# Kernel tuning notes

Hardware: AMD Instinct MI355X
Metric: run time of the kernel (lower is better)

The kernel has to match this reference:

```python
import jax, jax.numpy as jnp
import numpy as np

N_NODES = 100_000
N_EDGES = 1_600_000
IN_FEATS = 64
H_DIMS = 64
OUT_A = 2
OUT_B = 21
N_LAYERS = 2
EPS = 1e-5


def setup_inputs() -> dict:
    key = jax.random.key(0)
    ks = jax.random.split(key, 16)
    d = H_DIMS

    def rn(k, shape, scale=0.05):
        return jax.random.normal(k, shape, dtype=jnp.float32) * scale

    return {
        "v": jax.random.normal(ks[0], (N_NODES, IN_FEATS), dtype=jnp.float32),
        "src": jax.random.randint(ks[1], (N_EDGES,), 0, N_NODES),
        "dst": jax.random.randint(ks[2], (N_EDGES,), 0, N_NODES),
        "rel_type": jax.random.randint(ks[3], (N_EDGES,), 0, 3),
        "norm": jax.random.uniform(ks[4], (N_EDGES,), dtype=jnp.float32),
        "emb_W": rn(ks[5], (d, IN_FEATS)),
        "emb_b": jnp.zeros((d,), jnp.float32),
        "emb_gamma": jnp.ones((d,), jnp.float32),
        "emb_beta": jnp.zeros((d,), jnp.float32),
        "rel_weight": rn(ks[6], (3, d, d)),
        "gru_Wih": rn(ks[7], (3 * d, d)),
        "gru_Whh": rn(ks[8], (3 * d, d)),
        "gru_bih": jnp.zeros((3 * d,), jnp.float32),
        "gru_bhh": jnp.zeros((3 * d,), jnp.float32),
        "ker_gamma": jnp.ones((d,), jnp.float32),
        "ker_beta": jnp.zeros((d,), jnp.float32),
        "a_W1": rn(ks[9], (d, d)), "a_b1": jnp.zeros((d,), jnp.float32),
        "a_gamma": jnp.ones((d,), jnp.float32), "a_beta": jnp.zeros((d,), jnp.float32),
        "a_W2": rn(ks[10], (OUT_A, d)), "a_b2": jnp.zeros((OUT_A,), jnp.float32),
        "b_W1": rn(ks[11], (d, d)), "b_b1": jnp.zeros((d,), jnp.float32),
        "b_gamma": jnp.ones((d,), jnp.float32), "b_beta": jnp.zeros((d,), jnp.float32),
        "b_W2": rn(ks[12], (OUT_B, d)), "b_b2": jnp.zeros((OUT_B,), jnp.float32),
    }


def _bn(x, gamma, beta):
    # BatchNorm1d in training mode: batch statistics, biased variance
    mu = jnp.mean(x, axis=0)
    var = jnp.var(x, axis=0)
    return (x - mu) * jax.lax.rsqrt(var + EPS) * gamma + beta


def _gru_cell(x, h, Wih, Whh, bih, bhh):
    # torch nn.GRU single layer, gate order (r, z, n)
    gi = x @ Wih.T + bih
    gh = h @ Whh.T + bhh
    ir, iz, inn = jnp.split(gi, 3, axis=-1)
    hr, hz, hn = jnp.split(gh, 3, axis=-1)
    r = jax.nn.sigmoid(ir + hr)
    z = jax.nn.sigmoid(iz + hz)
    n = jnp.tanh(inn + r * hn)
    return (1.0 - z) * n + z * h


def reference(v, src, dst, rel_type, norm, emb_W, emb_b, emb_gamma, emb_beta,
              rel_weight, gru_Wih, gru_Whh, gru_bih, gru_bhh, ker_gamma, ker_beta,
              a_W1, a_b1, a_gamma, a_beta, a_W2, a_b2,
              b_W1, b_b1, b_gamma, b_beta, b_W2, b_b2):
    # Embedding: Linear -> BN -> ReLU
    h0 = jax.nn.relu(_bn(v @ emb_W.T + emb_b, emb_gamma, emb_beta))
    output = h0
    h = jnp.zeros_like(h0)
    n_nodes = v.shape[0]
    for _ in range(N_LAYERS):
        # per-node relational transform for all 3 relations: [N, 3, d]
        x3 = jnp.einsum('nd,rdk->nrk', output, rel_weight)
        msg = x3[src, rel_type] * norm[:, None]                     # [E, d]
        swh = jax.ops.segment_sum(msg, dst, num_segments=n_nodes)   # [N, d]
        h = _gru_cell(swh, h, gru_Wih, gru_Whh, gru_bih, gru_bhh)
        output = h
    hk = _bn(output, ker_gamma, ker_beta)
    # task heads: Linear -> BN -> ReLU -> Linear (MLP with h_layers=2)
    xa = jax.nn.relu(_bn(hk @ a_W1.T + a_b1, a_gamma, a_beta)) @ a_W2.T + a_b2
    xb = jax.nn.relu(_bn(hk @ b_W1.T + b_b1, b_gamma, b_beta)) @ b_W2.T + b_b2
    return xa, xb
```

## Files before the change

### kernel.cpp

```cpp
#include <hip/hip_runtime.h>

#define NN 100000
#define NE 1600000
#define NP 100096
#define NBKT 391
#define CAP 6144
#define EPSV 1e-5f

typedef unsigned int u32;
typedef unsigned short u16;
typedef unsigned long long u64;
typedef __bf16 bf16x8 __attribute__((ext_vector_type(8)));
typedef float f32x4 __attribute__((ext_vector_type(4)));

#define GLBP(x) ((const __attribute__((address_space(1))) u32*)(x))
#define LDSP(x) ((__attribute__((address_space(3))) u32*)(x))

__device__ __forceinline__ u16 f2bf(float f) {
  u32 x = __float_as_uint(f);
  return (u16)((x + 0x7FFFu + ((x >> 16) & 1u)) >> 16);
}
__device__ __forceinline__ float bf2f(u16 h) { return __uint_as_float(((u32)h) << 16); }

__device__ __forceinline__ void pack_one(const float* W, u32* out, int K, int KOT, int i) {
  int q = i & 3, lane = (i >> 2) & 63, f = i >> 8;
  int ks = f / KOT, ot = f - ks * KOT;
  int o = ot * 16 + (lane & 15);
  int k = ks * 32 + (lane >> 4) * 8 + q * 2;
  out[i] = (u32)f2bf(W[o * K + k]) | ((u32)f2bf(W[o * K + k + 1]) << 16);
}

__global__ void setupA(const float* __restrict__ relw, const float* __restrict__ Wih,
                       const float* __restrict__ embW, const float* __restrict__ Whh,
                       float* __restrict__ Wrow, u32* __restrict__ PWem, u32* __restrict__ PWhh) {
  int b = blockIdx.x;
  if (b < 144) {
    int t = b * 256 + threadIdx.x;
    if (t >= 192 * 192) return;
    int kg = t / 192, j = t % 192;
    const float* a = relw + (j >> 6) * 4096 + (j & 63) * 64;
    const float* w = Wih + kg * 64;
    float s = 0.f;
#pragma unroll
    for (int k = 0; k < 64; ++k) s += a[k] * w[k];
    Wrow[kg * 192 + j] = s;
  } else if (b < 152) {
    pack_one(embW, PWem, 64, 4, (b - 144) * 256 + threadIdx.x);
  } else {
    pack_one(Whh, PWhh, 64, 12, (b - 152) * 256 + threadIdx.x);
  }
}

__global__ void pack_wf(const float* __restrict__ Wrow, u32* __restrict__ PWf) {
  pack_one(Wrow, PWf, 192, 12, blockIdx.x * 256 + threadIdx.x);
}

__global__ void fold_pack(const float* __restrict__ Wa, const float* __restrict__ Wb,
                          const float* __restrict__ kacc, const float* __restrict__ kg,
                          u32* __restrict__ P) {
  int i = blockIdx.x * 256 + threadIdx.x;
  int q = i & 3, lane = (i >> 2) & 63, f = i >> 8;
  int ks = f >> 3, ot = f & 7;
  int o = ot * 16 + (lane & 15);
  int k = ks * 32 + (lane >> 4) * 8 + q * 2;
  const float* W = (o < 64) ? (Wa + o * 64) : (Wb + (o - 64) * 64);
  const float inv = 1.f / NN;
  float m0 = kacc[k] * inv;
  float s0 = kg[k] * rsqrtf(kacc[64 + k] * inv - m0 * m0 + EPSV);
  float m1 = kacc[k + 1] * inv;
  float s1 = kg[k + 1] * rsqrtf(kacc[64 + k + 1] * inv - m1 * m1 + EPSV);
  P[i] = (u32)f2bf(W[k] * s0) | ((u32)f2bf(W[k + 1] * s1) << 16);
}

__global__ __launch_bounds__(256) void countplace(const int* __restrict__ src,
                                                  const int* __restrict__ dst,
                                                  const int* __restrict__ rt,
                                                  const float* __restrict__ nrm,
                                                  int* __restrict__ gcnt,
                                                  u64* __restrict__ region) {
  __shared__ u32 hist[NBKT], gbase[NBKT];
  const int t = threadIdx.x;
  for (int i = t; i < NBKT; i += 256) hist[i] = 0;
  __syncthreads();
  const int e0 = blockIdx.x * 2048 + t;
  u32 rlo[8], rhi[8], lrank[8];
  int bkt[8];
#pragma unroll
  for (int i = 0; i < 8; ++i) {
    int e = e0 + i * 256;
    bkt[i] = -1;
    if (e < NE) {
      int d = dst[e];
      int b = d >> 8;
      bkt[i] = b;
      lrank[i] = atomicAdd(&hist[b], 1u);
      rlo[i] = (u32)src[e] | ((u32)rt[e] << 20) | ((u32)(d & 255) << 22);
      rhi[i] = __float_as_uint(nrm[e]);
    }
  }
  __syncthreads();
  for (int i = t; i < NBKT; i += 256) {
    u32 h = hist[i];
    gbase[i] = h ? (u32)atomicAdd(&gcnt[i], (int)h) : 0u;
  }
  __syncthreads();
#pragma unroll
  for (int i = 0; i < 8; ++i) {
    if (bkt[i] >= 0) {
      u32 pos = gbase[bkt[i]] + lrank[i];
      if (pos < CAP)
        region[(size_t)bkt[i] * CAP + pos] = (u64)rlo[i] | ((u64)rhi[i] << 32);
    }
  }
}

__global__ __launch_bounds__(512) void bucketscan(const int* __restrict__ gcnt,
                                                  int* __restrict__ bbase) {
  int t = threadIdx.x;
  int v = (t < NBKT) ? (gcnt[t] + 768) : 0;
  __shared__ int sh[512];
  sh[t] = v;
  __syncthreads();
#pragma unroll
  for (int off = 1; off < 512; off <<= 1) {
    int u = (t >= off) ? sh[t - off] : 0;
    __syncthreads();
    sh[t] += u;
    __syncthreads();
  }
  if (t < NBKT) bbase[t] = sh[t] - v;
}

__global__ __launch_bounds__(256) void localsort(const int* __restrict__ gcnt,
                                                 const int* __restrict__ bbase,
                                                 const u64* __restrict__ region,
                                                 u64* __restrict__ csr,
                                                 int* __restrict__ rowpr) {
  const int b = blockIdx.x, t = threadIdx.x;
  int n = gcnt[b];
  if (n > CAP) n = CAP;
  const int base = bbase[b];
  __shared__ u32 hist[1024], sc[256];
#pragma unroll
  for (int i = 0; i < 4; ++i) hist[t + 256 * i] = 0;
  __syncthreads();
  for (int i = t; i < n; i += 256)
    atomicAdd(&hist[(u32)(region[(size_t)b * CAP + i] >> 20) & 1023u], 1u);
  __syncthreads();
  u32 a0 = hist[4 * t], a1 = hist[4 * t + 1], a2 = hist[4 * t + 2];
  u32 p0 = (a0 + 1) & ~1u, p1 = (a1 + 1) & ~1u, p2 = (a2 + 1) & ~1u;
  u32 part = p0 + p1 + p2;
  sc[t] = part;
  __syncthreads();
#pragma unroll
  for (int off = 1; off < 256; off <<= 1) {
    u32 u = (t >= off) ? sc[t - off] : 0;
    __syncthreads();
    sc[t] += u;
    __syncthreads();
  }
  u32 ex = sc[t] - part;
  int node = b * 256 + t;
  rowpr[4 * node + 0] = base + (int)ex;
  rowpr[4 * node + 1] = base + (int)(ex + p0);
  rowpr[4 * node + 2] = base + (int)(ex + p0 + p1);
  rowpr[4 * node + 3] = base + (int)(ex + p0 + p1 + p2);
  __syncthreads();
  hist[4 * t + 0] = ex;
  hist[4 * t + 1] = ex + p0;
  hist[4 * t + 2] = ex + p0 + p1;
  __syncthreads();
  for (int i = t; i < n; i += 256) {
    u64 rec = region[(size_t)b * CAP + i];
    u32 pos = atomicAdd(&hist[(u32)(rec >> 20) & 1023u], 1u);
    csr[(size_t)base + pos] = rec;
  }
  __syncthreads();
  if (a0 & 1) csr[(size_t)base + ex + a0] = 0ull;
  if (a1 & 1) csr[(size_t)base + ex + p0 + a1] = 0ull;
  if (a2 & 1) csr[(size_t)base + ex + p0 + p1 + a2] = 0ull;
}

__global__ __launch_bounds__(256) void csr_gather(const int* __restrict__ rowpr,
                                                  const u64* __restrict__ csr,
                                                  const u16* __restrict__ Xbf,
                                                  u16* __restrict__ ACCbf) {
  int wv = blockIdx.x * 4 + (threadIdx.x >> 6);
  int lane = threadIdx.x & 63;
  if (wv >= NN) return;
  const int half = lane >> 5, c2 = lane & 31;
  int4 rp = *reinterpret_cast<const int4*>(rowpr + 4 * wv);
  const int b0 = __builtin_amdgcn_readfirstlane(rp.x);
  const int b1 = __builtin_amdgcn_readfirstlane(rp.y);
  const int b2 = __builtin_amdgcn_readfirstlane(rp.z);
  const int b3 = __builtin_amdgcn_readfirstlane(rp.w);
  const u32* X4 = (const u32*)Xbf;
  float a0x = 0.f, a0y = 0.f, a1x = 0.f, a1y = 0.f, a2x = 0.f, a2y = 0.f;
#define PAIRB(J, AX, AY)                                                        \
  { u32 sA = (u32)__builtin_amdgcn_readlane((int)lo, (J));                      \
    u32 sB = (u32)__builtin_amdgcn_readlane((int)lo, (J) + 1);                  \
    u32 nA = (u32)__builtin_amdgcn_readlane((int)hi, (J));                      \
    u32 nB = (u32)__builtin_amdgcn_readlane((int)hi, (J) + 1);                  \
    u32 srp = half ? sB : sA;                                                   \
    float nm = __uint_as_float(half ? nB : nA);                                 \
    u32 xw = X4[((srp & 0xFFFFFu) << 5) | (u32)c2];                             \
    AX = fmaf(__uint_as_float(xw << 16), nm, AX);                               \
    AY = fmaf(__uint_as_float(xw & 0xFFFF0000u), nm, AY); }
  for (int c = b0; c < b3; c += 64) {
    int m = b3 - c; m = m > 64 ? 64 : m;
    u32 lo = 0, hi = 0;
    if (lane < m) {
      u64 rec = csr[(size_t)c + lane];
      lo = (u32)rec; hi = (u32)(rec >> 32);
    }
    int j1 = b1 - c; j1 = j1 < 0 ? 0 : (j1 > m ? m : j1);
    int j2 = b2 - c; j2 = j2 < 0 ? 0 : (j2 > m ? m : j2);
    int j = 0;
    for (; j + 4 <= j1; j += 4) { PAIRB(j, a0x, a0y) PAIRB(j + 2, a0x, a0y) }
    if (j < j1) { PAIRB(j, a0x, a0y) j += 2; }
    for (; j + 4 <= j2; j += 4) { PAIRB(j, a1x, a1y) PAIRB(j + 2, a1x, a1y) }
    if (j < j2) { PAIRB(j, a1x, a1y) j += 2; }
    for (; j + 4 <= m; j += 4) { PAIRB(j, a2x, a2y) PAIRB(j + 2, a2x, a2y) }
    if (j < m) { PAIRB(j, a2x, a2y) j += 2; }
  }
#undef PAIRB
  a0x += __shfl_xor(a0x, 32); a0y += __shfl_xor(a0y, 32);
  a1x += __shfl_xor(a1x, 32); a1y += __shfl_xor(a1y, 32);
  a2x += __shfl_xor(a2x, 32); a2y += __shfl_xor(a2y, 32);
  if (half == 0) {
    u32* orow = (u32*)(ACCbf + (size_t)wv * 192);
    orow[c2]      = (u32)f2bf(a0x) | ((u32)f2bf(a0y) << 16);
    orow[32 + c2] = (u32)f2bf(a1x) | ((u32)f2bf(a1y) << 16);
    orow[64 + c2] = (u32)f2bf(a2x) | ((u32)f2bf(a2y) << 16);
  }
}

template<int K, int KO, int AF32, int GRU, int CS, int OUTBF>
__global__ __launch_bounds__(256) void gemm_mfma(
    const void* __restrict__ Av, const u32* __restrict__ Wpk, void* __restrict__ Yv,
    const float* __restrict__ bih, const float* __restrict__ bhh,
    const u16* __restrict__ G2B, const u16* __restrict__ Hv,
    float* __restrict__ csum, int n) {
  constexpr int KOT = KO / 16, KS = K / 32;
  constexpr int NFRAG = KS * KOT;
  __shared__ u32 bsh[NFRAG * 256];
  __shared__ float cs[2 * KO];
  const int lane = threadIdx.x & 63, w = threadIdx.x >> 6;
  const int rr = lane & 15, kg = lane >> 4;
  const long mbase = (long)blockIdx.x * 128 + w * 32;
  const u16* Abf = (const u16*)Av;
  const float* Af = (const float*)Av;

  bf16x8 abf[KS][2];
  float4 araw[AF32 ? KS : 1][2][2];
  if (AF32) {
#pragma unroll
    for (int ks = 0; ks < KS; ++ks)
#pragma unroll
      for (int hh = 0; hh < 2; ++hh) {
        long r = mbase + hh * 16 + rr;
        if (r > n - 1) r = n - 1;
        const float* pp = Af + r * K + ks * 32 + kg * 8;
        araw[ks][hh][0] = *(const float4*)pp;
        araw[ks][hh][1] = *(const float4*)(pp + 4);
      }
  } else {
#pragma unroll
    for (int ks = 0; ks < KS; ++ks)
#pragma unroll
      for (int hh = 0; hh < 2; ++hh)
        abf[ks][hh] = *reinterpret_cast<const bf16x8*>(
            Abf + (mbase + hh * 16 + rr) * K + ks * 32 + kg * 8);
  }

  constexpr int PASSES = NFRAG / 4;
#pragma unroll
  for (int i = 0; i < PASSES; ++i) {
    int c = i * 4 + w;
    __builtin_amdgcn_global_load_lds(GLBP(Wpk + (long)c * 256 + lane * 4),
                                     LDSP(&bsh[c * 256]), 16, 0, 0);
  }
  __syncthreads();

  if (AF32) {
#pragma unroll
    for (int ks = 0; ks < KS; ++ks)
#pragma unroll
      for (int hh = 0; hh < 2; ++hh) {
        float4 u0 = araw[ks][hh][0], u1 = araw[ks][hh][1];
        bf16x8 o_;
        o_[0] = __builtin_bit_cast(__bf16, f2bf(u0.x));
        o_[1] = __builtin_bit_cast(__bf16, f2bf(u0.y));
        o_[2] = __builtin_bit_cast(__bf16, f2bf(u0.z));
        o_[3] = __builtin_bit_cast(__bf16, f2bf(u0.w));
        o_[4] = __builtin_bit_cast(__bf16, f2bf(u1.x));
        o_[5] = __builtin_bit_cast(__bf16, f2bf(u1.y));
        o_[6] = __builtin_bit_cast(__bf16, f2bf(u1.z));
        o_[7] = __builtin_bit_cast(__bf16, f2bf(u1.w));
        abf[ks][hh] = o_;
      }
  }

  f32x4 acc[2][KOT] = {};
#pragma unroll
  for (int ks = 0; ks < KS; ++ks) {
#pragma unroll
    for (int o = 0; o < KOT; ++o) {
      bf16x8 bfr = *reinterpret_cast<const bf16x8*>(&bsh[((ks * KOT + o) * 64 + lane) * 4]);
      acc[0][o] = __builtin_amdgcn_mfma_f32_16x16x32_bf16(abf[ks][0], bfr, acc[0][o], 0, 0, 0);
      acc[1][o] = __builtin_amdgcn_mfma_f32_16x16x32_bf16(abf[ks][1], bfr, acc[1][o], 0, 0, 0);
    }
  }

  float s[KOT] = {}, ss[KOT] = {};
  if (GRU == 0) {
#pragma unroll
    for (int tl = 0; tl < 2; ++tl)
#pragma unroll
      for (int o = 0; o < KOT; ++o)
#pragma unroll
        for (int q = 0; q < 4; ++q) {
          long row = mbase + tl * 16 + kg * 4 + q;
          float vv = acc[tl][o][q];
          if (row < n) {
            long off = row * KO + o * 16 + rr;
            if (OUTBF) ((u16*)Yv)[off] = f2bf(vv);
            else       ((float*)Yv)[off] = vv;
            if (CS) { s[o] += vv; ss[o] += vv * vv; }
          }
        }
  } else {
    float bi[12], bh_[12];
#pragma unroll
    for (int g = 0; g < 3; ++g)
#pragma unroll
      for (int o = 0; o < 4; ++o) {
        bi[g * 4 + o] = bih[g * 64 + o * 16 + rr];
        bh_[g * 4 + o] = bhh[g * 64 + o * 16 + rr];
      }
#pragma unroll
    for (int tl = 0; tl < 2; ++tl)
#pragma unroll
      for (int o = 0; o < 4; ++o) {
        int c = o * 16 + rr;
#pragma unroll
        for (int q = 0; q < 4; ++q) {
          long row = mbase + tl * 16 + kg * 4 + q;
          float ir = acc[tl][o][q] + bi[o];
          float iz = acc[tl][o + 4][q] + bi[4 + o];
          float in_ = acc[tl][o + 8][q] + bi[8 + o];
          float hr = bh_[o], hz = bh_[4 + o], hn = bh_[8 + o], hv = 0.f;
          if (GRU == 2) {
            const u16* g2 = G2B + row * 192;
            hr += bf2f(g2[c]); hz += bf2f(g2[64 + c]); hn += bf2f(g2[128 + c]);
            hv = bf2f(Hv[row * 64 + c]);
          }
          float rg = 1.f / (1.f + __expf(-(ir + hr)));
          float zg = 1.f / (1.f + __expf(-(iz + hz)));
          float ng = tanhf(in_ + rg * hn);
          float h = (1.f - zg) * ng + (GRU == 2 ? zg * hv : 0.f);
          if (row < n) {
            ((u16*)Yv)[row * 64 + c] = f2bf(h);
            if (CS) { s[o] += h; ss[o] += h * h; }
          }
        }
      }
  }
  if (CS) {
    constexpr int LIM = (GRU == 0) ? 2 * KO : 128;
    constexpr int CKO = (GRU == 0) ? KO : 64;
    constexpr int OL = (GRU == 0) ? KOT : 4;
    for (int i = threadIdx.x; i < LIM; i += 256) cs[i] = 0.f;
    __syncthreads();
#pragma unroll
    for (int o = 0; o < OL; ++o) {
      int c = o * 16 + rr;
      atomicAdd(&cs[c], s[o]);
      atomicAdd(&cs[CKO + c], ss[o]);
    }
    __syncthreads();
    for (int i = threadIdx.x; i < LIM; i += 256) atomicAdd(&csum[i], cs[i]);
  }
}

__global__ __launch_bounds__(256) void bn_apply_bf(const float* __restrict__ X,
                                                   u16* __restrict__ Y,
                                                   const float* __restrict__ accs,
                                                   const float* __restrict__ gamma,
                                                   const float* __restrict__ beta, int relu) {
  __shared__ float scsh[128];
  int t = threadIdx.x;
  if (t < 64) {
    float mean = accs[t] * (1.f / NN);
    float var = accs[64 + t] * (1.f / NN) - mean * mean;
    float sc = gamma[t] * rsqrtf(var + EPSV);
    scsh[t] = sc;
    scsh[64 + t] = beta[t] - mean * sc;
  }
  __syncthreads();
  long i = (long)blockIdx.x * 256 + t;
  float4 v = reinterpret_cast<const float4*>(X)[i];
  int c = (int)((i * 4) & 63);
  v.x = fmaf(v.x, scsh[c],     scsh[64 + c]);
  v.y = fmaf(v.y, scsh[c + 1], scsh[65 + c]);
  v.z = fmaf(v.z, scsh[c + 2], scsh[66 + c]);
  v.w = fmaf(v.w, scsh[c + 3], scsh[67 + c]);
  if (relu) {
    v.x = fmaxf(v.x, 0.f); v.y = fmaxf(v.y, 0.f);
    v.z = fmaxf(v.z, 0.f); v.w = fmaxf(v.w, 0.f);
  }
  reinterpret_cast<ushort4*>(Y)[i] = make_ushort4(f2bf(v.x), f2bf(v.y), f2bf(v.z), f2bf(v.w));
}

template<int KO>
__global__ __launch_bounds__(256) void headfin_bn(const u16* __restrict__ Z,
                                                  const float* __restrict__ asum,
                                                  const float* __restrict__ asq,
                                                  const float* __restrict__ gamma,
                                                  const float* __restrict__ beta,
                                                  const float* __restrict__ W2,
                                                  const float* __restrict__ b2,
                                                  float* __restrict__ out, int n) {
  __shared__ float ws[KO * 64];
  __shared__ float scsh[128];
  int t = threadIdx.x;
  if (t < 64) {
    float mean = asum[t] * (1.f / NN);
    float var = asq[t] * (1.f / NN) - mean * mean;
    float sc = gamma[t] * rsqrtf(var + EPSV);
    scsh[t] = sc;
    scsh[64 + t] = beta[t] - mean * sc;
  }
  for (int i = t; i < KO * 64; i += 256) ws[i] = W2[i];
  __syncthreads();
  long node = (long)blockIdx.x * 256 + t;
  if (node >= n) return;
  const u16* zr = Z + node * 128;
  float x[64];
#pragma unroll
  for (int i = 0; i < 16; ++i) {
    ushort4 z4 = reinterpret_cast<const ushort4*>(zr)[i];
    int c = i * 4;
    x[c]     = fmaxf(fmaf(bf2f(z4.x), scsh[c],     scsh[64 + c]), 0.f);
    x[c + 1] = fmaxf(fmaf(bf2f(z4.y), scsh[c + 1], scsh[65 + c]), 0.f);
    x[c + 2] = fmaxf(fmaf(bf2f(z4.z), scsh[c + 2], scsh[66 + c]), 0.f);
    x[c + 3] = fmaxf(fmaf(bf2f(z4.w), scsh[c + 3], scsh[67 + c]), 0.f);
  }
#pragma unroll
  for (int o = 0; o < KO; ++o) {
    float a = b2[o];
#pragma unroll
    for (int d = 0; d < 64; ++d) a = fmaf(x[d], ws[o * 64 + d], a);
    out[node * KO + o] = a;
  }
}

extern "C" void kernel_launch(void* const* d_in, const int* in_sizes, int n_in,
                              void* d_out, int out_size, void* d_ws, size_t ws_size,
                              hipStream_t stream) {
  const float* v     = (const float*)d_in[0];
  const int*   src   = (const int*)d_in[1];
  const int*   dst   = (const int*)d_in[2];
  const int*   rt    = (const int*)d_in[3];
  const float* norm  = (const float*)d_in[4];
  const float* emb_W = (const float*)d_in[5];
  const float* emb_g  = (const float*)d_in[7];
  const float* emb_be = (const float*)d_in[8];
  const float* rel_w  = (const float*)d_in[9];
  const float* Wih    = (const float*)d_in[10];
  const float* Whh    = (const float*)d_in[11];
  const float* bih    = (const float*)d_in[12];
  const float* bhh    = (const float*)d_in[13];
  const float* ker_g  = (const float*)d_in[14];
  const float* aW1    = (const float*)d_in[16];
  const float* a_g  = (const float*)d_in[18];
  const float* a_be = (const float*)d_in[19];
  const float* aW2  = (const float*)d_in[20];
  const float* ab2  = (const float*)d_in[21];
  const float* bW1  = (const float*)d_in[22];
  const float* b_g  = (const float*)d_in[24];
  const float* b_be = (const float*)d_in[25];
  const float* bW2  = (const float*)d_in[26];
  const float* bb2  = (const float*)d_in[27];
  float* out = (float*)d_out;

  char* p = (char*)d_ws;
  auto nxt = [&](size_t bytes) -> char* {
    char* r = p; p += (bytes + 255) & ~(size_t)255; return r;
  };
  int*   GCNT = (int*)nxt(512 * 4);
  float* ACCs = (float*)nxt(512 * 4);
  float* Z    = (float*)nxt((size_t)NP * 64 * 4);
  u16*   X1   = (u16*)nxt((size_t)NP * 64 * 2);
  u16*   X2   = (u16*)nxt((size_t)NP * 64 * 2);
  u16*   ACCB = (u16*)nxt((size_t)NP * 192 * 2);
  u16*   G2B  = (u16*)nxt((size_t)NP * 192 * 2);
  u64*   REG  = (u64*)nxt((size_t)NBKT * CAP * 8);
  u64*   CSR  = (u64*)nxt((size_t)(NE + NBKT * 768 + 64) * 8);
  int*   BBAS = (int*)nxt(512 * 4);
  int*   ROWPR = (int*)nxt((size_t)(NP + 8) * 4 * 4);
  u32*   PWf  = (u32*)nxt(18432 * 4);
  u32*   PWem = (u32*)nxt(2048 * 4);
  u32*   PWhh = (u32*)nxt(6144 * 4);
  u32*   PWab = (u32*)nxt(4096 * 4);
  float* WROW = (float*)nxt(147456);

  hipMemsetAsync(GCNT, 0, 1024 * 4, stream);

  setupA<<<176, 256, 0, stream>>>(rel_w, Wih, emb_W, Whh, WROW, PWem, PWhh);
  countplace<<<782, 256, 0, stream>>>(src, dst, rt, norm, GCNT, REG);
  bucketscan<<<1, 512, 0, stream>>>(GCNT, BBAS);
  localsort<<<NBKT, 256, 0, stream>>>(GCNT, BBAS, REG, CSR, ROWPR);
  pack_wf<<<72, 256, 0, stream>>>(WROW, PWf);

  gemm_mfma<64, 64, 1, 0, 1, 0><<<782, 256, 0, stream>>>(v, PWem, Z, nullptr, nullptr,
                                                         nullptr, nullptr, ACCs + 0, NN);
  bn_apply_bf<<<6250, 256, 0, stream>>>(Z, X2, ACCs + 0, emb_g, emb_be, 1);

  csr_gather<<<25000, 256, 0, stream>>>(ROWPR, CSR, X2, ACCB);
  gemm_mfma<192, 192, 0, 1, 0, 1><<<782, 256, 0, stream>>>(ACCB, PWf, X1, bih, bhh,
                                                           nullptr, nullptr, nullptr, NN);

  csr_gather<<<25000, 256, 0, stream>>>(ROWPR, CSR, X1, ACCB);
  gemm_mfma<64, 192, 0, 0, 0, 1><<<782, 256, 0, stream>>>(X1, PWhh, G2B, nullptr, nullptr,
                                                          nullptr, nullptr, nullptr, NN);
  gemm_mfma<192, 192, 0, 2, 1, 1><<<782, 256, 0, stream>>>(ACCB, PWf, X1, bih, bhh,
                                                           G2B, X1, ACCs + 128, NN);

  fold_pack<<<16, 256, 0, stream>>>(aW1, bW1, ACCs + 128, ker_g, PWab);
  gemm_mfma<64, 128, 0, 0, 1, 1><<<782, 256, 0, stream>>>(X1, PWab, ACCB, nullptr, nullptr,
                                                          nullptr, nullptr, ACCs + 256, NN);
  headfin_bn<2><<<391, 256, 0, stream>>>((const u16*)ACCB, ACCs + 256, ACCs + 384,
                                         a_g, a_be, aW2, ab2, out, NN);
  headfin_bn<21><<<391, 256, 0, stream>>>((const u16*)ACCB + 64, ACCs + 320, ACCs + 448,
                                          b_g, b_be, bW2, bb2, out + (long)NN * 2, NN);
}
```

Measured before the change: 380.8 us.

## Fuse hidden-state GEMM into second-layer GRU GEMM via combined packed weight

Layer-2 GRU now runs one GEMM over the concatenated [aggregated messages | previous hidden] input, using a combined packed weight matrix of 256 output columns built by a new pack_comb kernel. The separate Whh GEMM and its G2B bf16 intermediate buffer go away, which removes one launch and a full write and read of an N×192 tensor. In addition, every GEMM block now uses 8 waves of 16 rows each instead of 4 waves of 32 rows. That raises thread count and occupancy but halves the reuse of each B fragment per wave and adds zero-padded MFMA work in the combined weight. X1 is read as the hidden input and written as the output in the same kernel, which stays safe only because each row is read before it is written by the same thread.

```diff
diff --git a/kernel.cpp b/kernel.cpp
--- a/kernel.cpp
+++ b/kernel.cpp
@@ -21,18 +21,21 @@
   return (u16)((x + 0x7FFFu + ((x >> 16) & 1u)) >> 16);
 }
 __device__ __forceinline__ float bf2f(u16 h) { return __uint_as_float(((u32)h) << 16); }
+__device__ __forceinline__ u32 pk2(float a, float b) {
+  return (u32)f2bf(a) | ((u32)f2bf(b) << 16);
+}
 
 __device__ __forceinline__ void pack_one(const float* W, u32* out, int K, int KOT, int i) {
   int q = i & 3, lane = (i >> 2) & 63, f = i >> 8;
   int ks = f / KOT, ot = f - ks * KOT;
   int o = ot * 16 + (lane & 15);
   int k = ks * 32 + (lane >> 4) * 8 + q * 2;
-  out[i] = (u32)f2bf(W[o * K + k]) | ((u32)f2bf(W[o * K + k + 1]) << 16);
+  out[i] = pk2(W[o * K + k], W[o * K + k + 1]);
 }
 
 __global__ void setupA(const float* __restrict__ relw, const float* __restrict__ Wih,
-                       const float* __restrict__ embW, const float* __restrict__ Whh,
-                       float* __restrict__ Wrow, u32* __restrict__ PWem, u32* __restrict__ PWhh) {
+                       const float* __restrict__ embW,
+                       float* __restrict__ Wrow, u32* __restrict__ PWem) {
   int b = blockIdx.x;
   if (b < 144) {
     int t = b * 256 + threadIdx.x;
@@ -44,15 +47,36 @@
 #pragma unroll
     for (int k = 0; k < 64; ++k) s += a[k] * w[k];
     Wrow[kg * 192 + j] = s;
-  } else if (b < 152) {
+  } else {
     pack_one(embW, PWem, 64, 4, (b - 144) * 256 + threadIdx.x);
-  } else {
-    pack_one(Whh, PWhh, 64, 12, (b - 152) * 256 + threadIdx.x);
   }
 }
 
 __global__ void pack_wf(const float* __restrict__ Wrow, u32* __restrict__ PWf) {
   pack_one(Wrow, PWf, 192, 12, blockIdx.x * 256 + threadIdx.x);
+}
+
+__global__ void pack_comb(const float* __restrict__ Wrow, const float* __restrict__ Whh,
+                          u32* __restrict__ P) {
+  int i = blockIdx.x * 256 + threadIdx.x;
+  int q = i & 3, lane = (i >> 2) & 63, f = i >> 8;
+  int ks = f >> 4, o = f & 15;
+  u32 val = 0u;
+  if (ks < 6) {
+    if (o < 12) {
+      int oo = o * 16 + (lane & 15);
+      int k = ks * 32 + (lane >> 4) * 8 + q * 2;
+      val = pk2(Wrow[oo * 192 + k], Wrow[oo * 192 + k + 1]);
+    }
+  } else {
+    int o2 = (o < 8) ? o : (o >= 12 ? o - 4 : -1);
+    if (o2 >= 0) {
+      int oo = o2 * 16 + (lane & 15);
+      int k = (ks - 6) * 32 + (lane >> 4) * 8 + q * 2;
+      val = pk2(Whh[oo * 64 + k], Whh[oo * 64 + k + 1]);
+    }
+  }
+  P[i] = val;
 }
 
 __global__ void fold_pack(const float* __restrict__ Wa, const float* __restrict__ Wb,
@@ -69,7 +93,7 @@
   float s0 = kg[k] * rsqrtf(kacc[64 + k] * inv - m0 * m0 + EPSV);
   float m1 = kacc[k + 1] * inv;
   float s1 = kg[k + 1] * rsqrtf(kacc[64 + k + 1] * inv - m1 * m1 + EPSV);
-  P[i] = (u32)f2bf(W[k] * s0) | ((u32)f2bf(W[k + 1] * s1) << 16);
+  P[i] = pk2(W[k] * s0, W[k + 1] * s1);
 }
 
 __global__ __launch_bounds__(256) void countplace(const int* __restrict__ src,
@@ -229,54 +253,54 @@
   a2x += __shfl_xor(a2x, 32); a2y += __shfl_xor(a2y, 32);
   if (half == 0) {
     u32* orow = (u32*)(ACCbf + (size_t)wv * 192);
-    orow[c2]      = (u32)f2bf(a0x) | ((u32)f2bf(a0y) << 16);
-    orow[32 + c2] = (u32)f2bf(a1x) | ((u32)f2bf(a1y) << 16);
-    orow[64 + c2] = (u32)f2bf(a2x) | ((u32)f2bf(a2y) << 16);
-  }
-}
-
-template<int K, int KO, int AF32, int GRU, int CS, int OUTBF>
-__global__ __launch_bounds__(256) void gemm_mfma(
-    const void* __restrict__ Av, const u32* __restrict__ Wpk, void* __restrict__ Yv,
-    const float* __restrict__ bih, const float* __restrict__ bhh,
-    const u16* __restrict__ G2B, const u16* __restrict__ Hv,
-    float* __restrict__ csum, int n) {
-  constexpr int KOT = KO / 16, KS = K / 32;
-  constexpr int NFRAG = KS * KOT;
+    orow[c2]      = pk2(a0x, a0y);
+    orow[32 + c2] = pk2(a1x, a1y);
+    orow[64 + c2] = pk2(a2x, a2y);
+  }
+}
+
+template<int K1, int K2, int KO, int AF32, int GRU, int CS, int OUTBF>
+__global__ __launch_bounds__(512) void gemm_mfma(
+    const void* __restrict__ Av, const u16* A2v, const u32* __restrict__ Wpk,
+    void* Yv, const float* __restrict__ bih, const float* __restrict__ bhh,
+    const u16* Hv, float* __restrict__ csum, int n) {
+  constexpr int KS1 = K1 / 32, KS2 = K2 / 32, KS = KS1 + KS2;
+  constexpr int KOT = KO / 16, NFRAG = KS * KOT;
+  constexpr int CSN = GRU ? 128 : 2 * KO;
   __shared__ u32 bsh[NFRAG * 256];
-  __shared__ float cs[2 * KO];
+  __shared__ float cs[CSN];
   const int lane = threadIdx.x & 63, w = threadIdx.x >> 6;
   const int rr = lane & 15, kg = lane >> 4;
-  const long mbase = (long)blockIdx.x * 128 + w * 32;
+  const long mbase = (long)blockIdx.x * 128 + w * 16;
   const u16* Abf = (const u16*)Av;
   const float* Af = (const float*)Av;
 
-  bf16x8 abf[KS][2];
-  float4 araw[AF32 ? KS : 1][2][2];
+  bf16x8 abf[KS];
+  float4 araw[AF32 ? KS1 : 1][2];
   if (AF32) {
-#pragma unroll
-    for (int ks = 0; ks < KS; ++ks)
-#pragma unroll
-      for (int hh = 0; hh < 2; ++hh) {
-        long r = mbase + hh * 16 + rr;
-        if (r > n - 1) r = n - 1;
-        const float* pp = Af + r * K + ks * 32 + kg * 8;
-        araw[ks][hh][0] = *(const float4*)pp;
-        araw[ks][hh][1] = *(const float4*)(pp + 4);
-      }
+    long r = mbase + rr;
+    if (r > n - 1) r = n - 1;
+#pragma unroll
+    for (int ks = 0; ks < KS1; ++ks) {
+      const float* pp = Af + r * K1 + ks * 32 + kg * 8;
+      araw[ks][0] = *(const float4*)pp;
+      araw[ks][1] = *(const float4*)(pp + 4);
+    }
   } else {
 #pragma unroll
-    for (int ks = 0; ks < KS; ++ks)
-#pragma unroll
-      for (int hh = 0; hh < 2; ++hh)
-        abf[ks][hh] = *reinterpret_cast<const bf16x8*>(
-            Abf + (mbase + hh * 16 + rr) * K + ks * 32 + kg * 8);
-  }
-
-  constexpr int PASSES = NFRAG / 4;
+    for (int ks = 0; ks < KS1; ++ks)
+      abf[ks] = *reinterpret_cast<const bf16x8*>(Abf + (mbase + rr) * K1 + ks * 32 + kg * 8);
+  }
+  if constexpr (KS2 > 0) {
+#pragma unroll
+    for (int ks = 0; ks < KS2; ++ks)
+      abf[KS1 + ks] = *reinterpret_cast<const bf16x8*>(A2v + (mbase + rr) * 64 + ks * 32 + kg * 8);
+  }
+
+  constexpr int PASSES = NFRAG / 8;
 #pragma unroll
   for (int i = 0; i < PASSES; ++i) {
-    int c = i * 4 + w;
+    int c = i * 8 + w;
     __builtin_amdgcn_global_load_lds(GLBP(Wpk + (long)c * 256 + lane * 4),
                                      LDSP(&bsh[c * 256]), 16, 0, 0);
   }
@@ -284,51 +308,46 @@
 
   if (AF32) {
 #pragma unroll
-    for (int ks = 0; ks < KS; ++ks)
-#pragma unroll
-      for (int hh = 0; hh < 2; ++hh) {
-        float4 u0 = araw[ks][hh][0], u1 = araw[ks][hh][1];
-        bf16x8 o_;
-        o_[0] = __builtin_bit_cast(__bf16, f2bf(u0.x));
-        o_[1] = __builtin_bit_cast(__bf16, f2bf(u0.y));
-        o_[2] = __builtin_bit_cast(__bf16, f2bf(u0.z));
-        o_[3] = __builtin_bit_cast(__bf16, f2bf(u0.w));
-        o_[4] = __builtin_bit_cast(__bf16, f2bf(u1.x));
-        o_[5] = __builtin_bit_cast(__bf16, f2bf(u1.y));
-        o_[6] = __builtin_bit_cast(__bf16, f2bf(u1.z));
-        o_[7] = __builtin_bit_cast(__bf16, f2bf(u1.w));
-        abf[ks][hh] = o_;
-      }
-  }
-
-  f32x4 acc[2][KOT] = {};
+    for (int ks = 0; ks < KS1; ++ks) {
+      float4 u0 = araw[ks][0], u1 = araw[ks][1];
+      bf16x8 o_;
+      o_[0] = __builtin_bit_cast(__bf16, f2bf(u0.x));
+      o_[1] = __builtin_bit_cast(__bf16, f2bf(u0.y));
+      o_[2] = __builtin_bit_cast(__bf16, f2bf(u0.z));
+      o_[3] = __builtin_bit_cast(__bf16, f2bf(u0.w));
+      o_[4] = __builtin_bit_cast(__bf16, f2bf(u1.x));
+      o_[5] = __builtin_bit_cast(__bf16, f2bf(u1.y));
+      o_[6] = __builtin_bit_cast(__bf16, f2bf(u1.z));
+      o_[7] = __builtin_bit_cast(__bf16, f2bf(u1.w));
+      abf[ks] = o_;
+    }
+  }
+
+  f32x4 acc[KOT] = {};
 #pragma unroll
   for (int ks = 0; ks < KS; ++ks) {
 #pragma unroll
     for (int o = 0; o < KOT; ++o) {
       bf16x8 bfr = *reinterpret_cast<const bf16x8*>(&bsh[((ks * KOT + o) * 64 + lane) * 4]);
-      acc[0][o] = __builtin_amdgcn_mfma_f32_16x16x32_bf16(abf[ks][0], bfr, acc[0][o], 0, 0, 0);
-      acc[1][o] = __builtin_amdgcn_mfma_f32_16x16x32_bf16(abf[ks][1], bfr, acc[1][o], 0, 0, 0);
+      acc[o] = __builtin_amdgcn_mfma_f32_16x16x32_bf16(abf[ks], bfr, acc[o], 0, 0, 0);
     }
   }
 
   float s[KOT] = {}, ss[KOT] = {};
   if (GRU == 0) {
 #pragma unroll
-    for (int tl = 0; tl < 2; ++tl)
-#pragma unroll
-      for (int o = 0; o < KOT; ++o)
-#pragma unroll
-        for (int q = 0; q < 4; ++q) {
-          long row = mbase + tl * 16 + kg * 4 + q;
-          float vv = acc[tl][o][q];
-          if (row < n) {
-            long off = row * KO + o * 16 + rr;
-            if (OUTBF) ((u16*)Yv)[off] = f2bf(vv);
-            else       ((float*)Yv)[off] = vv;
-            if (CS) { s[o] += vv; ss[o] += vv * vv; }
-          }
+    for (int o = 0; o < KOT; ++o)
+#pragma unroll
+      for (int q = 0; q < 4; ++q) {
+        long row = mbase + kg * 4 + q;
+        float vv = acc[o][q];
+        if (row < n) {
+          long off = row * KO + o * 16 + rr;
+          if (OUTBF) ((u16*)Yv)[off] = f2bf(vv);
+          else       ((float*)Yv)[off] = vv;
+          if (CS) { s[o] += vv; ss[o] += vv * vv; }
         }
+      }
   } else {
     float bi[12], bh_[12];
 #pragma unroll
@@ -339,38 +358,33 @@
         bh_[g * 4 + o] = bhh[g * 64 + o * 16 + rr];
       }
 #pragma unroll
-    for (int tl = 0; tl < 2; ++tl)
-#pragma unroll
-      for (int o = 0; o < 4; ++o) {
-        int c = o * 16 + rr;
-#pragma unroll
-        for (int q = 0; q < 4; ++q) {
-          long row = mbase + tl * 16 + kg * 4 + q;
-          float ir = acc[tl][o][q] + bi[o];
-          float iz = acc[tl][o + 4][q] + bi[4 + o];
-          float in_ = acc[tl][o + 8][q] + bi[8 + o];
-          float hr = bh_[o], hz = bh_[4 + o], hn = bh_[8 + o], hv = 0.f;
-          if (GRU == 2) {
-            const u16* g2 = G2B + row * 192;
-            hr += bf2f(g2[c]); hz += bf2f(g2[64 + c]); hn += bf2f(g2[128 + c]);
-            hv = bf2f(Hv[row * 64 + c]);
-          }
-          float rg = 1.f / (1.f + __expf(-(ir + hr)));
-          float zg = 1.f / (1.f + __expf(-(iz + hz)));
-          float ng = tanhf(in_ + rg * hn);
-          float h = (1.f - zg) * ng + (GRU == 2 ? zg * hv : 0.f);
-          if (row < n) {
-            ((u16*)Yv)[row * 64 + c] = f2bf(h);
-            if (CS) { s[o] += h; ss[o] += h * h; }
-          }
+    for (int o = 0; o < 4; ++o) {
+      int c = o * 16 + rr;
+#pragma unroll
+      for (int q = 0; q < 4; ++q) {
+        long row = mbase + kg * 4 + q;
+        float rg = 1.f / (1.f + __expf(-(acc[o][q] + bi[o] + bh_[o])));
+        float zg = 1.f / (1.f + __expf(-(acc[o + 4][q] + bi[4 + o] + bh_[4 + o])));
+        float h;
+        if (GRU == 1) {
+          float ng = tanhf(acc[o + 8][q] + bi[8 + o] + rg * bh_[8 + o]);
+          h = (1.f - zg) * ng;
+        } else {
+          float ng = tanhf(acc[o + 8][q] + bi[8 + o] + rg * (acc[o + 12][q] + bh_[8 + o]));
+          float hv = bf2f(Hv[row * 64 + c]);
+          h = (1.f - zg) * ng + zg * hv;
+        }
+        if (row < n) {
+          ((u16*)Yv)[row * 64 + c] = f2bf(h);
+          if (CS) { s[o] += h; ss[o] += h * h; }
         }
       }
+    }
   }
   if (CS) {
-    constexpr int LIM = (GRU == 0) ? 2 * KO : 128;
-    constexpr int CKO = (GRU == 0) ? KO : 64;
-    constexpr int OL = (GRU == 0) ? KOT : 4;
-    for (int i = threadIdx.x; i < LIM; i += 256) cs[i] = 0.f;
+    constexpr int CKO = GRU ? 64 : KO;
+    constexpr int OL = GRU ? 4 : KOT;
+    for (int i = threadIdx.x; i < CSN; i += 512) cs[i] = 0.f;
     __syncthreads();
 #pragma unroll
     for (int o = 0; o < OL; ++o) {
@@ -379,7 +393,7 @@
       atomicAdd(&cs[CKO + c], ss[o]);
     }
     __syncthreads();
-    for (int i = threadIdx.x; i < LIM; i += 256) atomicAdd(&csum[i], cs[i]);
+    for (int i = threadIdx.x; i < CSN; i += 512) atomicAdd(&csum[i], cs[i]);
   }
 }
 
@@ -494,42 +508,40 @@
   u16*   X1   = (u16*)nxt((size_t)NP * 64 * 2);
   u16*   X2   = (u16*)nxt((size_t)NP * 64 * 2);
   u16*   ACCB = (u16*)nxt((size_t)NP * 192 * 2);
-  u16*   G2B  = (u16*)nxt((size_t)NP * 192 * 2);
   u64*   REG  = (u64*)nxt((size_t)NBKT * CAP * 8);
   u64*   CSR  = (u64*)nxt((size_t)(NE + NBKT * 768 + 64) * 8);
   int*   BBAS = (int*)nxt(512 * 4);
   int*   ROWPR = (int*)nxt((size_t)(NP + 8) * 4 * 4);
   u32*   PWf  = (u32*)nxt(18432 * 4);
+  u32*   PWC  = (u32*)nxt(32768 * 4);
   u32*   PWem = (u32*)nxt(2048 * 4);
-  u32*   PWhh = (u32*)nxt(6144 * 4);
   u32*   PWab = (u32*)nxt(4096 * 4);
   float* WROW = (float*)nxt(147456);
 
   hipMemsetAsync(GCNT, 0, 1024 * 4, stream);
 
-  setupA<<<176, 256, 0, stream>>>(rel_w, Wih, emb_W, Whh, WROW, PWem, PWhh);
+  setupA<<<152, 256, 0, stream>>>(rel_w, Wih, emb_W, WROW, PWem);
   countplace<<<782, 256, 0, stream>>>(src, dst, rt, norm, GCNT, REG);
   bucketscan<<<1, 512, 0, stream>>>(GCNT, BBAS);
   localsort<<<NBKT, 256, 0, stream>>>(GCNT, BBAS, REG, CSR, ROWPR);
   pack_wf<<<72, 256, 0, stream>>>(WROW, PWf);
-
-  gemm_mfma<64, 64, 1, 0, 1, 0><<<782, 256, 0, stream>>>(v, PWem, Z, nullptr, nullptr,
-                                                         nullptr, nullptr, ACCs + 0, NN);
+  pack_comb<<<128, 256, 0, stream>>>(WROW, Whh, PWC);
+
+  gemm_mfma<64, 0, 64, 1, 0, 1, 0><<<782, 512, 0, stream>>>(
+      v, nullptr, PWem, Z, nullptr, nullptr, nullptr, ACCs + 0, NN);
   bn_apply_bf<<<6250, 256, 0, stream>>>(Z, X2, ACCs + 0, emb_g, emb_be, 1);
 
   csr_gather<<<25000, 256, 0, stream>>>(ROWPR, CSR, X2, ACCB);
-  gemm_mfma<192, 192, 0, 1, 0, 1><<<782, 256, 0, stream>>>(ACCB, PWf, X1, bih, bhh,
-                                                           nullptr, nullptr, nullptr, NN);
+  gemm_mfma<192, 0, 192, 0, 1, 0, 1><<<782, 512, 0, stream>>>(
+      ACCB, nullptr, PWf, X1, bih, bhh, nullptr, nullptr, NN);
 
   csr_gather<<<25000, 256, 0, stream>>>(ROWPR, CSR, X1, ACCB);
-  gemm_mfma<64, 192, 0, 0, 0, 1><<<782, 256, 0, stream>>>(X1, PWhh, G2B, nullptr, nullptr,
-                                                          nullptr, nullptr, nullptr, NN);
-  gemm_mfma<192, 192, 0, 2, 1, 1><<<782, 256, 0, stream>>>(ACCB, PWf, X1, bih, bhh,
-                                                           G2B, X1, ACCs + 128, NN);
+  gemm_mfma<192, 64, 256, 0, 2, 1, 1><<<782, 512, 0, stream>>>(
+      ACCB, X1, PWC, X1, bih, bhh, X1, ACCs + 128, NN);
 
   fold_pack<<<16, 256, 0, stream>>>(aW1, bW1, ACCs + 128, ker_g, PWab);
-  gemm_mfma<64, 128, 0, 0, 1, 1><<<782, 256, 0, stream>>>(X1, PWab, ACCB, nullptr, nullptr,
-                                                          nullptr, nullptr, ACCs + 256, NN);
+  gemm_mfma<64, 0, 128, 0, 0, 1, 1><<<782, 512, 0, stream>>>(
+      X1, nullptr, PWab, ACCB, nullptr, nullptr, nullptr, ACCs + 256, NN);
   headfin_bn<2><<<391, 256, 0, stream>>>((const u16*)ACCB, ACCs + 256, ACCs + 384,
                                          a_g, a_be, aW2, ab2, out, NN);
   headfin_bn<21><<<391, 256, 0, stream>>>((const u16*)ACCB + 64, ACCs + 320, ACCs + 448,
```

Measured after the change: 397.7 us. 4.4% more time.
